# Optimization experiments

Hardware: AMD Instinct MI355X
Metric: run time of the kernel (lower is better)

## Reference

```python
import jax, jax.numpy as jnp
import numpy as np

B, CTX, QST, E, H = 8, 4096, 512, 300, 128

def setup_inputs() -> dict:
    key = jax.random.key(0)
    k1, k2, k3, k4 = jax.random.split(key, 4)
    context_sequence = jax.random.normal(k1, (B, CTX, E), dtype=jnp.float32)
    question_sequence = jax.random.normal(k2, (B, QST, E), dtype=jnp.float32)
    question_mask = jnp.ones((B, QST), dtype=jnp.int32)
    # dense layer params (PyTorch Linear: y = x @ W.T + b)
    bound = 1.0 / np.sqrt(E)
    W = jax.random.uniform(k3, (H, E), minval=-bound, maxval=bound, dtype=jnp.float32)
    b = jax.random.uniform(k4, (H,), minval=-bound, maxval=bound, dtype=jnp.float32)
    return {"context_sequence": context_sequence, "question_sequence": question_sequence,
            "question_mask": question_mask, "W": W, "b": b}

def reference(context_sequence, question_sequence, question_mask, W, b):
    # ReLU(dense(x)) for both sequences
    ctx_logits = jax.nn.relu(jnp.einsum('bce,he->bch', context_sequence, W) + b)   # [B, CTX, H]
    qst_logits = jax.nn.relu(jnp.einsum('bqe,he->bqh', question_sequence, W) + b)  # [B, QST, H]
    scores = jnp.einsum('bch,bqh->bcq', ctx_logits, qst_logits)                    # [B, CTX, QST]
    scores = jnp.where(question_mask[:, None, :] == 0, -jnp.inf, scores)
    attn = jax.nn.softmax(scores, axis=-1)
    return jnp.einsum('bcq,bqh->bch', attn, qst_logits)                            # [B, CTX, H]
```

## Files before the change

### kernel.cpp

```cpp
#include <hip/hip_runtime.h>
#include <hip/hip_bf16.h>

#define BB   8
#define SCTX 4096
#define SQ   512
#define EE   300
#define HH   128
#define EP   320
#define CST  328
#define QCH  136
#define LOG2E 1.4426950408889634f

typedef short short8 __attribute__((ext_vector_type(8)));
typedef float f32x4  __attribute__((ext_vector_type(4)));

#define MFMA16(a, b, c) __builtin_amdgcn_mfma_f32_16x16x32_bf16((a), (b), (c), 0, 0, 0)

__device__ __forceinline__ short f2bf(float f) {
  unsigned u = __builtin_bit_cast(unsigned, f);
  u += 0x7fffu + ((u >> 16) & 1u);
  return (short)(u >> 16);
}
__device__ __forceinline__ float bf2f(short s) {
  return __builtin_bit_cast(float, ((unsigned)(unsigned short)s) << 16);
}

__global__ void k_wpad(const float* __restrict__ W, short* __restrict__ wsw) {
  const int h = blockIdx.x, k = threadIdx.x;
  float v = (k < EE) ? W[h * EE + k] : 0.0f;
  const int m = h >> 4, t = h & 15, kk = k >> 5, quad = (k >> 3) & 3, j = k & 7;
  wsw[((kk * 8 + m) * 64 + quad * 16 + t) * 8 + j] = f2bf(v);
}

__global__ __launch_bounds__(256) void k_qlog(const float* __restrict__ qst,
                                              const short* __restrict__ wsw,
                                              const float* __restrict__ bias,
                                              short* __restrict__ ql,
                                              short* __restrict__ qlT) {
  const int b = blockIdx.y;
  const int m0 = blockIdx.x * 32;
  const int tid = threadIdx.x;
  const int w = tid >> 6, l = tid & 63, t = l & 15, quad = l >> 4;
  const int g = w >> 1, hf = w & 1;

  __shared__ __align__(16) short cst[32 * CST];

  const float4* cbase = (const float4*)(qst + (size_t)(b * SQ + m0) * EE);
#pragma unroll
  for (int j = 0; j < 10; ++j) {
    int i4 = tid + j * 256;
    if (i4 < 2400) {
      float4 v = cbase[i4];
      int row = i4 / 75, c4 = i4 - row * 75;
      short* dp = cst + row * CST + c4 * 4;
      dp[0] = f2bf(v.x); dp[1] = f2bf(v.y); dp[2] = f2bf(v.z); dp[3] = f2bf(v.w);
    }
  }
  for (int i = tid; i < 320; i += 256) {
    int row = i / 10, c = (i - row * 10) * 2;
    cst[row * CST + 300 + c] = 0;
    cst[row * CST + 301 + c] = 0;
  }
  __syncthreads();

  const short* arow = cst + (g * 16 + t) * CST;
  f32x4 acc[4] = {};
#pragma unroll
  for (int kk = 0; kk < 10; ++kk) {
    const int k = kk * 32 + quad * 8;
    short8 a = *(const short8*)(arow + k);
#pragma unroll
    for (int n = 0; n < 4; ++n) {
      short8 w8 = *(const short8*)(wsw + ((kk * 8 + hf * 4 + n) * 64 + l) * 8);
      acc[n] = MFMA16(a, w8, acc[n]);
    }
  }
#pragma unroll
  for (int n = 0; n < 4; ++n) {
    const int h = (hf * 4 + n) * 16 + t;
    const float bv = bias[h];
#pragma unroll
    for (int r = 0; r < 4; ++r) {
      float v = fmaxf(acc[n][r] + bv, 0.0f);
      short s16 = f2bf(v);
      const int row = m0 + g * 16 + quad * 4 + r;
      ql[((size_t)b * SQ + row) * HH + h] = s16;
      qlT[((size_t)b * HH + h) * SQ + row] = s16;
    }
  }
}

__global__ __launch_bounds__(256, 2) void k_attn(const float* __restrict__ ctx,
                                                 const short* __restrict__ wsw,
                                                 const float* __restrict__ bias,
                                                 const int* __restrict__ mask,
                                                 const short* __restrict__ ql,
                                                 const short* __restrict__ qlT,
                                                 float* __restrict__ out) {
  const int b = blockIdx.y;
  const int m0 = blockIdx.x * 64;
  const int tid = threadIdx.x;
  const int w = tid >> 6, l = tid & 63, t = l & 15, quad = l >> 4;
  const int g = w >> 1, hf = w & 1;

  __shared__ __align__(16) short uq[17408];
  __shared__ __align__(16) short uc[8704];
  __shared__ short maskh[SQ];
  short* cst = uq;
  short* qch = uq;
  short* clt = uc;
  short* pbw = uc + w * 2176;

  const short8* qsrc = (const short8*)(ql + (size_t)b * SQ * HH);
  const short8* vsrc = (const short8*)(qlT + (size_t)b * HH * SQ);

  short8 sreg[8];
#pragma unroll
  for (int j = 0; j < 8; ++j) sreg[j] = qsrc[tid + j * 256];

  for (int i = tid; i < SQ; i += 256)
    maskh[i] = f2bf(mask[b * SQ + i] ? -8.0f : -1e30f);

  for (int i = 0; i < 2; ++i) {
    const float4* cbase = (const float4*)(ctx + ((size_t)b * SCTX + m0 + i * 32) * EE);
#pragma unroll
    for (int j = 0; j < 10; ++j) {
      int i4 = tid + j * 256;
      if (i4 < 2400) {
        float4 v = cbase[i4];
        int row = i4 / 75, c4 = i4 - row * 75;
        short* dp = cst + row * CST + c4 * 4;
        dp[0] = f2bf(v.x); dp[1] = f2bf(v.y); dp[2] = f2bf(v.z); dp[3] = f2bf(v.w);
      }
    }
    for (int k = tid; k < 320; k += 256) {
      int row = k / 10, c = (k - row * 10) * 2;
      cst[row * CST + 300 + c] = 0;
      cst[row * CST + 301 + c] = 0;
    }
    __syncthreads();
    const short* arow = cst + (g * 16 + t) * CST;
    f32x4 acc[4] = {};
#pragma unroll
    for (int kk = 0; kk < 10; ++kk) {
      const int k = kk * 32 + quad * 8;
      short8 a = *(const short8*)(arow + k);
#pragma unroll
      for (int n = 0; n < 4; ++n) {
        short8 w8 = *(const short8*)(wsw + ((kk * 8 + hf * 4 + n) * 64 + l) * 8);
        acc[n] = MFMA16(a, w8, acc[n]);
      }
    }
#pragma unroll
    for (int n = 0; n < 4; ++n) {
      const int h = (hf * 4 + n) * 16 + t;
      const float bv = bias[h];
#pragma unroll
      for (int r = 0; r < 4; ++r) {
        float v = fmaxf(acc[n][r] + bv, 0.0f);
        clt[(i * 32 + g * 16 + quad * 4 + r) * 136 + h] = f2bf(v);
      }
    }
    __syncthreads();
  }

  short8 af[4];
#pragma unroll
  for (int kk = 0; kk < 4; ++kk)
    af[kk] = *(const short8*)&clt[(w * 16 + t) * 136 + kk * 32 + quad * 8];
  __syncthreads();

  f32x4 o[8] = {};
  f32x4 rsum = {0.f, 0.f, 0.f, 0.f};
  for (int c = 0; c < 4; ++c) {
#pragma unroll
    for (int j = 0; j < 8; ++j) {
      int i = tid + j * 256;
      *(short8*)&qch[(i >> 4) * QCH + (i & 15) * 8] = sreg[j];
    }
    __syncthreads();
#pragma unroll
    for (int j = 0; j < 8; ++j) {
      int i = tid + j * 256;
      sreg[j] = vsrc[(i >> 4) * 64 + c * 16 + (i & 15)];
    }
#pragma unroll
    for (int n2 = 0; n2 < 8; ++n2) {
      f32x4 sv = {0.f, 0.f, 0.f, 0.f};
      const short* qrow = qch + (n2 * 16 + t) * QCH;
#pragma unroll
      for (int kk = 0; kk < 4; ++kk) {
        short8 b8 = *(const short8*)(qrow + kk * 32 + quad * 8);
        sv = MFMA16(af[kk], b8, sv);
      }
      const float mb = bf2f(maskh[c * 128 + n2 * 16 + t]);
#pragma unroll
      for (int r = 0; r < 4; ++r) {
        float p = exp2f((sv[r] + mb) * LOG2E);
        rsum[r] += p;
        pbw[(quad * 4 + r) * 136 + n2 * 16 + t] = f2bf(p);
      }
    }
    __syncthreads();
#pragma unroll
    for (int j = 0; j < 8; ++j) {
      int i = tid + j * 256;
      *(short8*)&qch[(i >> 4) * QCH + (i & 15) * 8] = sreg[j];
    }
    __syncthreads();
    if (c < 3) {
#pragma unroll
      for (int j = 0; j < 8; ++j)
        sreg[j] = qsrc[(c + 1) * 2048 + tid + j * 256];
    }
#pragma unroll
    for (int kk = 0; kk < 4; ++kk) {
      short8 pa = *(const short8*)&pbw[t * 136 + kk * 32 + quad * 8];
#pragma unroll
      for (int n = 0; n < 8; ++n) {
        short8 v8 = *(const short8*)&qch[(n * 16 + t) * QCH + kk * 32 + quad * 8];
        o[n] = MFMA16(pa, v8, o[n]);
      }
    }
    __syncthreads();
  }
#pragma unroll
  for (int off = 8; off; off >>= 1)
#pragma unroll
    for (int r = 0; r < 4; ++r) rsum[r] += __shfl_xor(rsum[r], off);

  f32x4 rinv;
#pragma unroll
  for (int r = 0; r < 4; ++r) rinv[r] = 1.0f / rsum[r];
  float* obase = out + ((size_t)b * SCTX + m0 + w * 16) * HH;
#pragma unroll
  for (int n = 0; n < 8; ++n)
#pragma unroll
    for (int r = 0; r < 4; ++r)
      obase[(quad * 4 + r) * HH + n * 16 + t] = o[n][r] * rinv[r];
}

extern "C" void kernel_launch(void* const* d_in, const int* in_sizes, int n_in,
                              void* d_out, int out_size, void* d_ws, size_t ws_size,
                              hipStream_t stream) {
  const float* ctx  = (const float*)d_in[0];
  const float* qst  = (const float*)d_in[1];
  const int*   mask = (const int*)d_in[2];
  const float* W    = (const float*)d_in[3];
  const float* bias = (const float*)d_in[4];
  float* out = (float*)d_out;

  short* wsw  = (short*)d_ws;
  short* ql   = (short*)((char*)d_ws + 81920);
  short* qlT  = ql + (size_t)BB * SQ * HH;

  k_wpad<<<dim3(HH), dim3(EP), 0, stream>>>(W, wsw);
  k_qlog<<<dim3(SQ / 32, BB), dim3(256), 0, stream>>>(qst, wsw, bias, ql, qlT);
  k_attn<<<dim3(SCTX / 64, BB), dim3(256), 0, stream>>>(ctx, wsw, bias, mask, ql, qlT, out);
}
```

Measured before the change: 122.6 us.

## Keep softmax probabilities in registers via transposed QK MFMA and lane shuffles

Computes the score tile transposed (question rows as the A operand) so the probabilities can be repacked into the PV MFMA A-operand with cross-lane shuffles instead of a round trip through LDS. It also stages Q and V chunks together in two LDS buffers, with both prefetched into registers one chunk ahead, which cuts the barriers per chunk from four to two. The cost is more LDS (the V buffer doubles in size, which may limit the two-blocks-per-CU occupancy), more registers for the dual prefetch, and extra shuffle and select instructions.

```diff
diff --git a/kernel.cpp b/kernel.cpp
--- a/kernel.cpp
+++ b/kernel.cpp
@@ -11,8 +11,10 @@
 #define QCH  136
 #define LOG2E 1.4426950408889634f
 
+typedef short bhalf4 __attribute__((ext_vector_type(4)));
 typedef short short8 __attribute__((ext_vector_type(8)));
 typedef float f32x4  __attribute__((ext_vector_type(4)));
+typedef unsigned u32x4 __attribute__((ext_vector_type(4)));
 
 #define MFMA16(a, b, c) __builtin_amdgcn_mfma_f32_16x16x32_bf16((a), (b), (c), 0, 0, 0)
 
@@ -23,6 +25,9 @@
 }
 __device__ __forceinline__ float bf2f(short s) {
   return __builtin_bit_cast(float, ((unsigned)(unsigned short)s) << 16);
+}
+__device__ __forceinline__ unsigned pack2(float a, float b) {
+  return (unsigned)(unsigned short)f2bf(a) | ((unsigned)(unsigned short)f2bf(b) << 16);
 }
 
 __global__ void k_wpad(const float* __restrict__ W, short* __restrict__ wsw) {
@@ -104,19 +109,23 @@
   const int g = w >> 1, hf = w & 1;
 
   __shared__ __align__(16) short uq[17408];
-  __shared__ __align__(16) short uc[8704];
+  __shared__ __align__(16) short uv[17408];
   __shared__ short maskh[SQ];
   short* cst = uq;
   short* qch = uq;
-  short* clt = uc;
-  short* pbw = uc + w * 2176;
+  short* clt = uv;
+  short* vch = uv;
 
   const short8* qsrc = (const short8*)(ql + (size_t)b * SQ * HH);
   const short8* vsrc = (const short8*)(qlT + (size_t)b * HH * SQ);
 
-  short8 sreg[8];
-#pragma unroll
-  for (int j = 0; j < 8; ++j) sreg[j] = qsrc[tid + j * 256];
+  short8 qreg[8], vreg[8];
+#pragma unroll
+  for (int j = 0; j < 8; ++j) {
+    int i = tid + j * 256;
+    qreg[j] = qsrc[i];
+    vreg[j] = vsrc[(i >> 4) * 64 + (i & 15)];
+  }
 
   for (int i = tid; i < SQ; i += 256)
     maskh[i] = f2bf(mask[b * SQ + i] ? -8.0f : -1e30f);
@@ -170,68 +179,84 @@
     af[kk] = *(const short8*)&clt[(w * 16 + t) * 136 + kk * 32 + quad * 8];
   __syncthreads();
 
+#pragma unroll
+  for (int j = 0; j < 8; ++j) {
+    int i = tid + j * 256;
+    *(short8*)&qch[(i >> 4) * QCH + (i & 15) * 8] = qreg[j];
+    *(short8*)&vch[(i >> 4) * QCH + (i & 15) * 8] = vreg[j];
+  }
+
+  const int srcA = ((quad & 1) * 2) * 16 + t;
+  const int srcB = srcA + 16;
+  const bool hiq = quad >= 2;
+
   f32x4 o[8] = {};
-  f32x4 rsum = {0.f, 0.f, 0.f, 0.f};
+  float rtot = 0.0f;
   for (int c = 0; c < 4; ++c) {
-#pragma unroll
-    for (int j = 0; j < 8; ++j) {
-      int i = tid + j * 256;
-      *(short8*)&qch[(i >> 4) * QCH + (i & 15) * 8] = sreg[j];
-    }
-    __syncthreads();
-#pragma unroll
-    for (int j = 0; j < 8; ++j) {
-      int i = tid + j * 256;
-      sreg[j] = vsrc[(i >> 4) * 64 + c * 16 + (i & 15)];
-    }
-#pragma unroll
-    for (int n2 = 0; n2 < 8; ++n2) {
-      f32x4 sv = {0.f, 0.f, 0.f, 0.f};
-      const short* qrow = qch + (n2 * 16 + t) * QCH;
-#pragma unroll
-      for (int kk = 0; kk < 4; ++kk) {
-        short8 b8 = *(const short8*)(qrow + kk * 32 + quad * 8);
-        sv = MFMA16(af[kk], b8, sv);
-      }
-      const float mb = bf2f(maskh[c * 128 + n2 * 16 + t]);
+    __syncthreads();
+    if (c < 3) {
+#pragma unroll
+      for (int j = 0; j < 8; ++j) {
+        int i = tid + j * 256;
+        qreg[j] = qsrc[(c + 1) * 2048 + i];
+        vreg[j] = vsrc[(i >> 4) * 64 + (c + 1) * 16 + (i & 15)];
+      }
+    }
+#pragma unroll
+    for (int kk = 0; kk < 4; ++kk) {
+      f32x4 svE = {0.f, 0.f, 0.f, 0.f}, svO = {0.f, 0.f, 0.f, 0.f};
+      const short* qrE = qch + ((kk * 2) * 16 + t) * QCH;
+      const short* qrO = qch + ((kk * 2 + 1) * 16 + t) * QCH;
+#pragma unroll
+      for (int kx = 0; kx < 4; ++kx) {
+        short8 b8e = *(const short8*)(qrE + kx * 32 + quad * 8);
+        short8 b8o = *(const short8*)(qrO + kx * 32 + quad * 8);
+        svE = MFMA16(b8e, af[kx], svE);
+        svO = MFMA16(b8o, af[kx], svO);
+      }
+      bhalf4 mbE = *(const bhalf4*)&maskh[c * 128 + (kk * 2) * 16 + quad * 4];
+      bhalf4 mbO = *(const bhalf4*)&maskh[c * 128 + (kk * 2 + 1) * 16 + quad * 4];
+      float pE[4], pO[4];
 #pragma unroll
       for (int r = 0; r < 4; ++r) {
-        float p = exp2f((sv[r] + mb) * LOG2E);
-        rsum[r] += p;
-        pbw[(quad * 4 + r) * 136 + n2 * 16 + t] = f2bf(p);
-      }
-    }
-    __syncthreads();
-#pragma unroll
-    for (int j = 0; j < 8; ++j) {
-      int i = tid + j * 256;
-      *(short8*)&qch[(i >> 4) * QCH + (i & 15) * 8] = sreg[j];
+        pE[r] = exp2f((svE[r] + bf2f(mbE[r])) * LOG2E);
+        pO[r] = exp2f((svO[r] + bf2f(mbO[r])) * LOG2E);
+        rtot += pE[r] + pO[r];
+      }
+      unsigned pkE0 = pack2(pE[0], pE[1]), pkE1 = pack2(pE[2], pE[3]);
+      unsigned pkO0 = pack2(pO[0], pO[1]), pkO1 = pack2(pO[2], pO[3]);
+      unsigned sE0 = (unsigned)__shfl((int)pkE0, srcA), sE1 = (unsigned)__shfl((int)pkE1, srcA);
+      unsigned sO0 = (unsigned)__shfl((int)pkO0, srcA), sO1 = (unsigned)__shfl((int)pkO1, srcA);
+      unsigned tE0 = (unsigned)__shfl((int)pkE0, srcB), tE1 = (unsigned)__shfl((int)pkE1, srcB);
+      unsigned tO0 = (unsigned)__shfl((int)pkO0, srcB), tO1 = (unsigned)__shfl((int)pkO1, srcB);
+      u32x4 av;
+      av[0] = hiq ? sO0 : sE0;
+      av[1] = hiq ? sO1 : sE1;
+      av[2] = hiq ? tO0 : tE0;
+      av[3] = hiq ? tO1 : tE1;
+      short8 pa = __builtin_bit_cast(short8, av);
+#pragma unroll
+      for (int n = 0; n < 8; ++n) {
+        short8 v8 = *(const short8*)&vch[(n * 16 + t) * QCH + kk * 32 + quad * 8];
+        o[n] = MFMA16(pa, v8, o[n]);
+      }
     }
     __syncthreads();
     if (c < 3) {
 #pragma unroll
-      for (int j = 0; j < 8; ++j)
-        sreg[j] = qsrc[(c + 1) * 2048 + tid + j * 256];
-    }
-#pragma unroll
-    for (int kk = 0; kk < 4; ++kk) {
-      short8 pa = *(const short8*)&pbw[t * 136 + kk * 32 + quad * 8];
-#pragma unroll
-      for (int n = 0; n < 8; ++n) {
-        short8 v8 = *(const short8*)&qch[(n * 16 + t) * QCH + kk * 32 + quad * 8];
-        o[n] = MFMA16(pa, v8, o[n]);
-      }
-    }
-    __syncthreads();
-  }
-#pragma unroll
-  for (int off = 8; off; off >>= 1)
-#pragma unroll
-    for (int r = 0; r < 4; ++r) rsum[r] += __shfl_xor(rsum[r], off);
-
+      for (int j = 0; j < 8; ++j) {
+        int i = tid + j * 256;
+        *(short8*)&qch[(i >> 4) * QCH + (i & 15) * 8] = qreg[j];
+        *(short8*)&vch[(i >> 4) * QCH + (i & 15) * 8] = vreg[j];
+      }
+    }
+  }
+
+  rtot += __shfl_xor(rtot, 16);
+  rtot += __shfl_xor(rtot, 32);
   f32x4 rinv;
 #pragma unroll
-  for (int r = 0; r < 4; ++r) rinv[r] = 1.0f / rsum[r];
+  for (int r = 0; r < 4; ++r) rinv[r] = 1.0f / __shfl(rtot, quad * 4 + r);
   float* obase = out + ((size_t)b * SCTX + m0 + w * 16) * HH;
 #pragma unroll
   for (int n = 0; n < 8; ++n)
```

Result: slower. 140.2 us (+14.4%).
